# Performance work log

Measured on AMD Instinct MI355X. Metric: run time of the kernel, lower is better.

The kernel has to match this reference:

```python
import jax, jax.numpy as jnp
import numpy as np

B, C, N, K = 2, 64, 20000, 16
COUT = 64


def setup_inputs() -> dict:
    key = jax.random.key(0)
    k1, k2, k3, k4, k5 = jax.random.split(key, 5)
    x = jax.random.normal(k1, (B, C, N, 1), dtype=jnp.float32)
    edge_index = jax.random.randint(k2, (2, B, N, K), 0, N)
    pos = jax.random.normal(k3, (B, 3, N, 1), dtype=jnp.float32)
    # BasicConv([2C, COUT]) -> 1x1 Conv2d weight [COUT, 2C] (+bias), then ReLU
    W = jax.random.normal(k4, (COUT, 2 * C), dtype=jnp.float32) * (1.0 / np.sqrt(2 * C))
    b = jax.random.normal(k5, (COUT,), dtype=jnp.float32) * 0.01
    return {"x": x, "edge_index": edge_index, "pos": pos, "W": W, "b": b}


def _gather(t, idx):
    # t: [B, C, N, 1], idx: [B, N, K] -> [B, C, N, K]
    t3 = t[..., 0]  # [B, C, N]
    return jax.vmap(lambda tb, ib: tb[:, ib])(t3, idx)


def reference(x, edge_index, pos, W, b):
    x_i = _gather(x, edge_index[1])           # [B, C, N, K] center
    x_j = _gather(x, edge_index[0])           # [B, C, N, K] neighbor
    feat = jnp.concatenate([x_i, x_j - x_i], axis=1)  # [B, 2C, N, K]
    # 1x1 conv + bias + ReLU
    out = jnp.einsum('oc,bcnk->bonk', W, feat) + b[None, :, None, None]
    out = jax.nn.relu(out)
    # distance-based suppression
    pos_i = _gather(pos, edge_index[1])       # [B, 3, N, K]
    pos_j = _gather(pos, edge_index[0])
    dis = jnp.sqrt(jnp.sum(jnp.square(pos_j - pos_i), axis=1))  # [B, N, K]
    suppression = 2.0 * jax.nn.sigmoid(-dis)[:, None, :, :]     # [B, 1, N, K]
    out = out * suppression
    max_value = jnp.max(out, axis=-1, keepdims=True)             # [B, COUT, N, 1]
    return max_value
```

## Files before the change

### kernel.cpp

```cpp
#include <hip/hip_runtime.h>
#include <math.h>

#define B_    2
#define C_    64
#define N_    20000
#define K_    16
#define COUT_ 64
#define TNC   64
#define NBC   ((N_ + TNC - 1) / TNC)
#define TN    16
#define NB    (N_ / TN)

typedef unsigned int   u32;
typedef unsigned short u16;
typedef __attribute__((ext_vector_type(8))) short bf16x8;
typedef __attribute__((ext_vector_type(4))) float f32x4;

static __device__ __forceinline__ u16 f2bf(float f) {
    union { float f; u32 u; } v; v.f = f;
    u32 r = (v.u + 0x7FFFu + ((v.u >> 16) & 1u)) >> 16;
    return (u16)r;
}
static __device__ __forceinline__ float uasf(u32 u) {
    union { u32 u; float f; } v; v.u = u; return v.f;
}
static __device__ __forceinline__ u32 bfsub2(u32 bv, u32 av) {
    float bl = uasf(bv << 16), bh = uasf(bv & 0xFFFF0000u);
    float al = uasf(av << 16), ah = uasf(av & 0xFFFF0000u);
    return (u32)f2bf(bl - al) | ((u32)f2bf(bh - ah) << 16);
}

#define SWZ(row, off) ((off) ^ (((row) & 7) << 4))

__global__ __launch_bounds__(256)
void precast(const float* __restrict__ x, const float* __restrict__ W,
             u16* __restrict__ xb, u16* __restrict__ wfrag) {
    const int bi = blockIdx.x;
    const int t  = threadIdx.x;

    if (bi == B_ * NBC) {
        const int l  = t & 63;
        const int ot = t >> 6;
        const int ro = (ot * 16 + (l & 15)) * 128 + ((l >> 4) << 3);
        #pragma unroll
        for (int ks = 0; ks < 4; ++ks) {
            u32 p[4];
            #pragma unroll
            for (int jj = 0; jj < 4; ++jj) {
                float v0 = W[ro + ks * 32 + 2 * jj];
                float v1 = W[ro + ks * 32 + 2 * jj + 1];
                p[jj] = (u32)f2bf(v0) | ((u32)f2bf(v1) << 16);
            }
            *(uint4*)&wfrag[(size_t)((ot * 4 + ks) * 64 + l) * 8] =
                make_uint4(p[0], p[1], p[2], p[3]);
        }
        return;
    }

    __shared__ float tile[64][68];
    const int b  = bi / NBC;
    const int n0 = (bi % NBC) * TNC;
    const float* xbase = x + (size_t)b * C_ * N_;
    #pragma unroll
    for (int r = 0; r < 4; ++r) {
        int flat = r * 256 + t;
        int c = flat >> 4, ng = (flat & 15) * 4;
        int n = n0 + ng;
        float4 v;
        if (n + 3 < N_) {
            v = *(const float4*)&xbase[c * N_ + n];
        } else {
            v.x = (n     < N_) ? xbase[c * N_ + n    ] : 0.0f;
            v.y = (n + 1 < N_) ? xbase[c * N_ + n + 1] : 0.0f;
            v.z = (n + 2 < N_) ? xbase[c * N_ + n + 2] : 0.0f;
            v.w = (n + 3 < N_) ? xbase[c * N_ + n + 3] : 0.0f;
        }
        *(float4*)&tile[c][ng] = v;
    }
    __syncthreads();

    const int n = t >> 2, q = t & 3;
    if (n0 + n < N_) {
        u32 p[8];
        #pragma unroll
        for (int jj = 0; jj < 8; ++jj) {
            float v0 = tile[q * 16 + 2 * jj][n];
            float v1 = tile[q * 16 + 2 * jj + 1][n];
            p[jj] = (u32)f2bf(v0) | ((u32)f2bf(v1) << 16);
        }
        u16* dst = xb + ((size_t)(b * N_ + n0 + n)) * 64 + q * 16;
        *(uint4*)dst       = make_uint4(p[0], p[1], p[2], p[3]);
        *(uint4*)(dst + 8) = make_uint4(p[4], p[5], p[6], p[7]);
    }
}

__global__ __launch_bounds__(256)
void fused(const int* __restrict__ ei, const float* __restrict__ pos,
           const u16* __restrict__ xb, const u16* __restrict__ wfrag,
           const float* __restrict__ bias, float* __restrict__ out) {
    __shared__ u16   feat[256 * 128];
    __shared__ uint2 esl[256];
    __shared__ float otile[16][66];

    const int bi   = blockIdx.x;
    const int b    = bi / NB;
    const int n0   = (bi % NB) * TN;
    const int t    = threadIdx.x;
    const int lane = t & 63;
    const int w    = t >> 6;
    const int g    = lane >> 4;

    {
        const int idx = n0 * K_ + t;
        int i0 = ei[(size_t)b * N_ * K_ + idx];
        int i1 = ei[((size_t)B_ + b) * N_ * K_ + idx];
        const float* pb = pos + (size_t)b * 3 * N_;
        float dx = pb[i0]          - pb[i1];
        float dy = pb[N_ + i0]     - pb[N_ + i1];
        float dz = pb[2 * N_ + i0] - pb[2 * N_ + i1];
        float dis = sqrtf(dx * dx + dy * dy + dz * dz);
        float s = 2.0f / (1.0f + __expf(dis));
        esl[t] = make_uint2((u32)i0 | ((u32)i1 << 16), __float_as_uint(s));
    }
    __syncthreads();

    {
        const uint4* xrow = (const uint4*)(xb + (size_t)b * N_ * 64);
        const int cq = t & 7;
        char* fb = (char*)feat;
        #pragma unroll
        for (int p = 0; p < 8; ++p) {
            int e = p * 32 + (t >> 3);
            uint2 ee = esl[e];
            int i0 = (int)(ee.x & 0xFFFFu);
            int i1 = (int)(ee.x >> 16);
            uint4 a  = xrow[((size_t)i1 << 3) + cq];
            uint4 bv = xrow[((size_t)i0 << 3) + cq];
            *(uint4*)(fb + SWZ(e, e * 256 + cq * 16)) = a;
            uint4 d;
            d.x = bfsub2(bv.x, a.x);
            d.y = bfsub2(bv.y, a.y);
            d.z = bfsub2(bv.z, a.z);
            d.w = bfsub2(bv.w, a.w);
            *(uint4*)(fb + SWZ(e, e * 256 + 128 + cq * 16)) = d;
        }
    }

    bf16x8 wf[16];
    #pragma unroll
    for (int f = 0; f < 16; ++f)
        wf[f] = *(const bf16x8*)&wfrag[(size_t)(f * 64 + lane) * 8];

    const int col = lane & 15;
    const float bo0 = bias[col], bo1 = bias[16 + col],
                bo2 = bias[32 + col], bo3 = bias[48 + col];
    __syncthreads();

    const char* fb = (const char*)feat;
    #pragma unroll
    for (int it = 0; it < 4; ++it) {
        const int et  = it * 4 + w;
        const int row = et * 16 + col;
        const int rb  = row * 256 + g * 16;
        bf16x8 a0 = *(const bf16x8*)(fb + SWZ(row, rb));
        bf16x8 a1 = *(const bf16x8*)(fb + SWZ(row, rb + 64));
        bf16x8 a2 = *(const bf16x8*)(fb + SWZ(row, rb + 128));
        bf16x8 a3 = *(const bf16x8*)(fb + SWZ(row, rb + 192));
        f32x4 ac0 = {0,0,0,0}, ac1 = ac0, ac2 = ac0, ac3 = ac0;
        ac0 = __builtin_amdgcn_mfma_f32_16x16x32_bf16(a0, wf[0],  ac0, 0,0,0);
        ac0 = __builtin_amdgcn_mfma_f32_16x16x32_bf16(a1, wf[1],  ac0, 0,0,0);
        ac0 = __builtin_amdgcn_mfma_f32_16x16x32_bf16(a2, wf[2],  ac0, 0,0,0);
        ac0 = __builtin_amdgcn_mfma_f32_16x16x32_bf16(a3, wf[3],  ac0, 0,0,0);
        ac1 = __builtin_amdgcn_mfma_f32_16x16x32_bf16(a0, wf[4],  ac1, 0,0,0);
        ac1 = __builtin_amdgcn_mfma_f32_16x16x32_bf16(a1, wf[5],  ac1, 0,0,0);
        ac1 = __builtin_amdgcn_mfma_f32_16x16x32_bf16(a2, wf[6],  ac1, 0,0,0);
        ac1 = __builtin_amdgcn_mfma_f32_16x16x32_bf16(a3, wf[7],  ac1, 0,0,0);
        ac2 = __builtin_amdgcn_mfma_f32_16x16x32_bf16(a0, wf[8],  ac2, 0,0,0);
        ac2 = __builtin_amdgcn_mfma_f32_16x16x32_bf16(a1, wf[9],  ac2, 0,0,0);
        ac2 = __builtin_amdgcn_mfma_f32_16x16x32_bf16(a2, wf[10], ac2, 0,0,0);
        ac2 = __builtin_amdgcn_mfma_f32_16x16x32_bf16(a3, wf[11], ac2, 0,0,0);
        ac3 = __builtin_amdgcn_mfma_f32_16x16x32_bf16(a0, wf[12], ac3, 0,0,0);
        ac3 = __builtin_amdgcn_mfma_f32_16x16x32_bf16(a1, wf[13], ac3, 0,0,0);
        ac3 = __builtin_amdgcn_mfma_f32_16x16x32_bf16(a2, wf[14], ac3, 0,0,0);
        ac3 = __builtin_amdgcn_mfma_f32_16x16x32_bf16(a3, wf[15], ac3, 0,0,0);

        float m0 = 0.f, m1 = 0.f, m2 = 0.f, m3 = 0.f;
#define EPI(REG) { \
        float sv = uasf(esl[et * 16 + g * 4 + REG].y); \
        m0 = fmaxf(m0, fmaxf(ac0[REG] + bo0, 0.f) * sv); \
        m1 = fmaxf(m1, fmaxf(ac1[REG] + bo1, 0.f) * sv); \
        m2 = fmaxf(m2, fmaxf(ac2[REG] + bo2, 0.f) * sv); \
        m3 = fmaxf(m3, fmaxf(ac3[REG] + bo3, 0.f) * sv); }
        EPI(0) EPI(1) EPI(2) EPI(3)
#undef EPI
        m0 = fmaxf(m0, __shfl_xor(m0, 16)); m0 = fmaxf(m0, __shfl_xor(m0, 32));
        m1 = fmaxf(m1, __shfl_xor(m1, 16)); m1 = fmaxf(m1, __shfl_xor(m1, 32));
        m2 = fmaxf(m2, __shfl_xor(m2, 16)); m2 = fmaxf(m2, __shfl_xor(m2, 32));
        m3 = fmaxf(m3, __shfl_xor(m3, 16)); m3 = fmaxf(m3, __shfl_xor(m3, 32));
        if (lane < 16) {
            otile[et][col]      = m0;
            otile[et][16 + col] = m1;
            otile[et][32 + col] = m2;
            otile[et][48 + col] = m3;
        }
    }
    __syncthreads();

    #pragma unroll
    for (int r = 0; r < 4; ++r) {
        int flat = r * 256 + t;
        int o = flat >> 4, n2 = flat & 15;
        __builtin_nontemporal_store(otile[n2][o],
            &out[((size_t)b * COUT_ + o) * N_ + n0 + n2]);
    }
}

extern "C" void kernel_launch(void* const* d_in, const int* in_sizes, int n_in,
                              void* d_out, int out_size, void* d_ws, size_t ws_size,
                              hipStream_t stream) {
    const float* x    = (const float*)d_in[0];
    const int*   ei   = (const int*)  d_in[1];
    const float* pos  = (const float*)d_in[2];
    const float* W    = (const float*)d_in[3];
    const float* bias = (const float*)d_in[4];
    float*       out  = (float*)d_out;

    u16* xb    = (u16*)d_ws;
    u16* wfrag = xb + (size_t)B_ * N_ * 64;

    hipLaunchKernelGGL(precast, dim3(B_ * NBC + 1), dim3(256), 0, stream,
                       x, W, xb, wfrag);
    hipLaunchKernelGGL(fused, dim3(B_ * NB), dim3(256), 0, stream,
                       ei, pos, xb, wfrag, bias, out);
}
```

Baseline: 113.0 us.

## Fold edge-difference into precombined weights and gather features directly into registers

Rewrites W·[xi, xj−xi] as (W1−W2)·xi + W2·xj, precomputing the combined bf16 weight fragments in the precast kernel. The fused kernel then loads xi/xj rows straight from global memory into MFMA operands, dropping the 64KB shared feature tile, the per-element bf16 subtraction and a barrier. This should raise occupancy and cut LDS traffic. The cost is that gather loads are now issued per MFMA-lane layout rather than through a cooperative staging pass, with slightly different rounding.

```diff
diff --git a/kernel.cpp b/kernel.cpp
--- a/kernel.cpp
+++ b/kernel.cpp
@@ -24,13 +24,9 @@
 static __device__ __forceinline__ float uasf(u32 u) {
     union { u32 u; float f; } v; v.u = u; return v.f;
 }
-static __device__ __forceinline__ u32 bfsub2(u32 bv, u32 av) {
-    float bl = uasf(bv << 16), bh = uasf(bv & 0xFFFF0000u);
-    float al = uasf(av << 16), ah = uasf(av & 0xFFFF0000u);
-    return (u32)f2bf(bl - al) | ((u32)f2bf(bh - ah) << 16);
-}
-
-#define SWZ(row, off) ((off) ^ (((row) & 7) << 4))
+static __device__ __forceinline__ bf16x8 asbf(uint4 v) {
+    union { uint4 u; bf16x8 b; } c; c.u = v; return c.b;
+}
 
 __global__ __launch_bounds__(256)
 void precast(const float* __restrict__ x, const float* __restrict__ W,
@@ -41,18 +37,23 @@
     if (bi == B_ * NBC) {
         const int l  = t & 63;
         const int ot = t >> 6;
-        const int ro = (ot * 16 + (l & 15)) * 128 + ((l >> 4) << 3);
+        const int o  = ot * 16 + (l & 15);
+        const int cb = (l >> 4) << 3;
         #pragma unroll
-        for (int ks = 0; ks < 4; ++ks) {
-            u32 p[4];
+        for (int h = 0; h < 2; ++h) {
+            u32 p1[4], p2[4];
             #pragma unroll
             for (int jj = 0; jj < 4; ++jj) {
-                float v0 = W[ro + ks * 32 + 2 * jj];
-                float v1 = W[ro + ks * 32 + 2 * jj + 1];
-                p[jj] = (u32)f2bf(v0) | ((u32)f2bf(v1) << 16);
+                int c0 = h * 32 + cb + 2 * jj, c1 = c0 + 1;
+                float w1a = W[o * 128 + c0],      w1b = W[o * 128 + c1];
+                float w2a = W[o * 128 + 64 + c0], w2b = W[o * 128 + 64 + c1];
+                p1[jj] = (u32)f2bf(w1a - w2a) | ((u32)f2bf(w1b - w2b) << 16);
+                p2[jj] = (u32)f2bf(w2a)       | ((u32)f2bf(w2b)       << 16);
             }
-            *(uint4*)&wfrag[(size_t)((ot * 4 + ks) * 64 + l) * 8] =
-                make_uint4(p[0], p[1], p[2], p[3]);
+            *(uint4*)&wfrag[(size_t)((ot * 4 + h)     * 64 + l) * 8] =
+                make_uint4(p1[0], p1[1], p1[2], p1[3]);
+            *(uint4*)&wfrag[(size_t)((ot * 4 + 2 + h) * 64 + l) * 8] =
+                make_uint4(p2[0], p2[1], p2[2], p2[3]);
         }
         return;
     }
@@ -98,7 +99,6 @@
 void fused(const int* __restrict__ ei, const float* __restrict__ pos,
            const u16* __restrict__ xb, const u16* __restrict__ wfrag,
            const float* __restrict__ bias, float* __restrict__ out) {
-    __shared__ u16   feat[256 * 128];
     __shared__ uint2 esl[256];
     __shared__ float otile[16][66];
 
@@ -109,6 +109,7 @@
     const int lane = t & 63;
     const int w    = t >> 6;
     const int g    = lane >> 4;
+    const int col  = lane & 15;
 
     {
         const int idx = n0 * K_ + t;
@@ -122,71 +123,51 @@
         float s = 2.0f / (1.0f + __expf(dis));
         esl[t] = make_uint2((u32)i0 | ((u32)i1 << 16), __float_as_uint(s));
     }
-    __syncthreads();
-
-    {
-        const uint4* xrow = (const uint4*)(xb + (size_t)b * N_ * 64);
-        const int cq = t & 7;
-        char* fb = (char*)feat;
-        #pragma unroll
-        for (int p = 0; p < 8; ++p) {
-            int e = p * 32 + (t >> 3);
-            uint2 ee = esl[e];
-            int i0 = (int)(ee.x & 0xFFFFu);
-            int i1 = (int)(ee.x >> 16);
-            uint4 a  = xrow[((size_t)i1 << 3) + cq];
-            uint4 bv = xrow[((size_t)i0 << 3) + cq];
-            *(uint4*)(fb + SWZ(e, e * 256 + cq * 16)) = a;
-            uint4 d;
-            d.x = bfsub2(bv.x, a.x);
-            d.y = bfsub2(bv.y, a.y);
-            d.z = bfsub2(bv.z, a.z);
-            d.w = bfsub2(bv.w, a.w);
-            *(uint4*)(fb + SWZ(e, e * 256 + 128 + cq * 16)) = d;
-        }
-    }
 
     bf16x8 wf[16];
     #pragma unroll
     for (int f = 0; f < 16; ++f)
         wf[f] = *(const bf16x8*)&wfrag[(size_t)(f * 64 + lane) * 8];
-
-    const int col = lane & 15;
     const float bo0 = bias[col], bo1 = bias[16 + col],
                 bo2 = bias[32 + col], bo3 = bias[48 + col];
     __syncthreads();
 
-    const char* fb = (const char*)feat;
+    const uint4* xrow = (const uint4*)(xb + (size_t)b * N_ * 64);
+
     #pragma unroll
     for (int it = 0; it < 4; ++it) {
-        const int et  = it * 4 + w;
-        const int row = et * 16 + col;
-        const int rb  = row * 256 + g * 16;
-        bf16x8 a0 = *(const bf16x8*)(fb + SWZ(row, rb));
-        bf16x8 a1 = *(const bf16x8*)(fb + SWZ(row, rb + 64));
-        bf16x8 a2 = *(const bf16x8*)(fb + SWZ(row, rb + 128));
-        bf16x8 a3 = *(const bf16x8*)(fb + SWZ(row, rb + 192));
+        const int nt = it * 4 + w;
+        uint2 ee = esl[nt * 16 + col];
+        int   i0 = (int)(ee.x & 0xFFFFu);
+        int   i1 = (int)(ee.x >> 16);
+        const uint4* ri = xrow + ((size_t)i1 << 3);
+        const uint4* rj = xrow + ((size_t)i0 << 3);
+        bf16x8 xi_lo = asbf(ri[g]);
+        bf16x8 xi_hi = asbf(ri[4 + g]);
+        bf16x8 xj_lo = asbf(rj[g]);
+        bf16x8 xj_hi = asbf(rj[4 + g]);
+
         f32x4 ac0 = {0,0,0,0}, ac1 = ac0, ac2 = ac0, ac3 = ac0;
-        ac0 = __builtin_amdgcn_mfma_f32_16x16x32_bf16(a0, wf[0],  ac0, 0,0,0);
-        ac0 = __builtin_amdgcn_mfma_f32_16x16x32_bf16(a1, wf[1],  ac0, 0,0,0);
-        ac0 = __builtin_amdgcn_mfma_f32_16x16x32_bf16(a2, wf[2],  ac0, 0,0,0);
-        ac0 = __builtin_amdgcn_mfma_f32_16x16x32_bf16(a3, wf[3],  ac0, 0,0,0);
-        ac1 = __builtin_amdgcn_mfma_f32_16x16x32_bf16(a0, wf[4],  ac1, 0,0,0);
-        ac1 = __builtin_amdgcn_mfma_f32_16x16x32_bf16(a1, wf[5],  ac1, 0,0,0);
-        ac1 = __builtin_amdgcn_mfma_f32_16x16x32_bf16(a2, wf[6],  ac1, 0,0,0);
-        ac1 = __builtin_amdgcn_mfma_f32_16x16x32_bf16(a3, wf[7],  ac1, 0,0,0);
-        ac2 = __builtin_amdgcn_mfma_f32_16x16x32_bf16(a0, wf[8],  ac2, 0,0,0);
-        ac2 = __builtin_amdgcn_mfma_f32_16x16x32_bf16(a1, wf[9],  ac2, 0,0,0);
-        ac2 = __builtin_amdgcn_mfma_f32_16x16x32_bf16(a2, wf[10], ac2, 0,0,0);
-        ac2 = __builtin_amdgcn_mfma_f32_16x16x32_bf16(a3, wf[11], ac2, 0,0,0);
-        ac3 = __builtin_amdgcn_mfma_f32_16x16x32_bf16(a0, wf[12], ac3, 0,0,0);
-        ac3 = __builtin_amdgcn_mfma_f32_16x16x32_bf16(a1, wf[13], ac3, 0,0,0);
-        ac3 = __builtin_amdgcn_mfma_f32_16x16x32_bf16(a2, wf[14], ac3, 0,0,0);
-        ac3 = __builtin_amdgcn_mfma_f32_16x16x32_bf16(a3, wf[15], ac3, 0,0,0);
+        ac0 = __builtin_amdgcn_mfma_f32_16x16x32_bf16(xi_lo, wf[0],  ac0, 0,0,0);
+        ac0 = __builtin_amdgcn_mfma_f32_16x16x32_bf16(xi_hi, wf[1],  ac0, 0,0,0);
+        ac0 = __builtin_amdgcn_mfma_f32_16x16x32_bf16(xj_lo, wf[2],  ac0, 0,0,0);
+        ac0 = __builtin_amdgcn_mfma_f32_16x16x32_bf16(xj_hi, wf[3],  ac0, 0,0,0);
+        ac1 = __builtin_amdgcn_mfma_f32_16x16x32_bf16(xi_lo, wf[4],  ac1, 0,0,0);
+        ac1 = __builtin_amdgcn_mfma_f32_16x16x32_bf16(xi_hi, wf[5],  ac1, 0,0,0);
+        ac1 = __builtin_amdgcn_mfma_f32_16x16x32_bf16(xj_lo, wf[6],  ac1, 0,0,0);
+        ac1 = __builtin_amdgcn_mfma_f32_16x16x32_bf16(xj_hi, wf[7],  ac1, 0,0,0);
+        ac2 = __builtin_amdgcn_mfma_f32_16x16x32_bf16(xi_lo, wf[8],  ac2, 0,0,0);
+        ac2 = __builtin_amdgcn_mfma_f32_16x16x32_bf16(xi_hi, wf[9],  ac2, 0,0,0);
+        ac2 = __builtin_amdgcn_mfma_f32_16x16x32_bf16(xj_lo, wf[10], ac2, 0,0,0);
+        ac2 = __builtin_amdgcn_mfma_f32_16x16x32_bf16(xj_hi, wf[11], ac2, 0,0,0);
+        ac3 = __builtin_amdgcn_mfma_f32_16x16x32_bf16(xi_lo, wf[12], ac3, 0,0,0);
+        ac3 = __builtin_amdgcn_mfma_f32_16x16x32_bf16(xi_hi, wf[13], ac3, 0,0,0);
+        ac3 = __builtin_amdgcn_mfma_f32_16x16x32_bf16(xj_lo, wf[14], ac3, 0,0,0);
+        ac3 = __builtin_amdgcn_mfma_f32_16x16x32_bf16(xj_hi, wf[15], ac3, 0,0,0);
 
         float m0 = 0.f, m1 = 0.f, m2 = 0.f, m3 = 0.f;
 #define EPI(REG) { \
-        float sv = uasf(esl[et * 16 + g * 4 + REG].y); \
+        float sv = uasf(esl[nt * 16 + g * 4 + REG].y); \
         m0 = fmaxf(m0, fmaxf(ac0[REG] + bo0, 0.f) * sv); \
         m1 = fmaxf(m1, fmaxf(ac1[REG] + bo1, 0.f) * sv); \
         m2 = fmaxf(m2, fmaxf(ac2[REG] + bo2, 0.f) * sv); \
@@ -198,10 +179,10 @@
         m2 = fmaxf(m2, __shfl_xor(m2, 16)); m2 = fmaxf(m2, __shfl_xor(m2, 32));
         m3 = fmaxf(m3, __shfl_xor(m3, 16)); m3 = fmaxf(m3, __shfl_xor(m3, 32));
         if (lane < 16) {
-            otile[et][col]      = m0;
-            otile[et][16 + col] = m1;
-            otile[et][32 + col] = m2;
-            otile[et][48 + col] = m3;
+            otile[nt][col]      = m0;
+            otile[nt][16 + col] = m1;
+            otile[nt][32 + col] = m2;
+            otile[nt][48 + col] = m3;
         }
     }
     __syncthreads();
```

Result: faster. 110.7 us (-2.0%).
